# Optimization experiments

Hardware: AMD Instinct MI355X
Metric: run time of the kernel (lower is better)

Reference implementation:

```python
import jax, jax.numpy as jnp
import numpy as np

HEAD_DIM = 64
N_HEADS = 64
N_KV = 8
Q_MULT = N_HEADS // N_KV  # 8
HIDDEN = 2880
SLIDING_WINDOW = 128
BASE = 150000.0
INIT_CTX = 4096
SCALING = 32.0
NTK_ALPHA = 1.0   # beta_slow
NTK_BETA = 32.0   # beta_fast
EPS = 1e-5
SM_SCALE = 1.0 / np.sqrt(HEAD_DIM)


def _cos_sin(num_tokens):
    # YaRN-style NTK rope (scaling_factor > 1 branch)
    freq = BASE ** (jnp.arange(0, HEAD_DIM, 2, dtype=jnp.float32) / HEAD_DIM)
    concentration = 0.1 * np.log(SCALING) + 1.0
    d_half = HEAD_DIM // 2
    low = d_half * np.log(INIT_CTX / (NTK_BETA * 2 * np.pi)) / np.log(BASE)
    high = d_half * np.log(INIT_CTX / (NTK_ALPHA * 2 * np.pi)) / np.log(BASE)
    interpolation = 1.0 / (SCALING * freq)
    extrapolation = 1.0 / freq
    ramp = (jnp.arange(d_half, dtype=jnp.float32) - low) / (high - low)
    mask = 1.0 - jnp.clip(ramp, 0.0, 1.0)
    inv_freq = interpolation * (1.0 - mask) + extrapolation * mask
    t = jnp.arange(num_tokens, dtype=jnp.float32)
    freqs = t[:, None] * inv_freq[None, :]  # [n, d/2]
    return jnp.cos(freqs) * concentration, jnp.sin(freqs) * concentration


def _apply_rotary(x, cos, sin):
    # x: [n, h, d]; cos/sin: [n, d/2]
    cos = cos[:, None, :].astype(x.dtype)
    sin = sin[:, None, :].astype(x.dtype)
    x1, x2 = jnp.split(x, 2, axis=-1)
    return jnp.concatenate((x1 * cos - x2 * sin, x2 * cos + x1 * sin), axis=-1)


def _forward(x, norm_w, qkv_w, out_w, sinks):
    b, s, h = x.shape  # b=1
    n = b * s
    # RMSNorm
    var = jnp.mean(jnp.square(x), axis=-1, keepdims=True)
    t = x * jax.lax.rsqrt(var + EPS) * norm_w
    # QKV projection
    qkv = jnp.einsum('bsh,hf->bsf', t, qkv_w)
    q_dim = N_HEADS * HEAD_DIM
    kv_dim = N_KV * HEAD_DIM
    q = qkv[:, :, :q_dim].reshape(n, N_KV, Q_MULT, HEAD_DIM)
    k = qkv[:, :, q_dim:q_dim + kv_dim].reshape(n, N_KV, HEAD_DIM)
    v = qkv[:, :, q_dim + kv_dim:].reshape(n, N_KV, HEAD_DIM)
    # RoPE
    cos, sin = _cos_sin(n)
    q = _apply_rotary(q.reshape(n, -1, HEAD_DIM), cos, sin).reshape(n, N_KV, Q_MULT, HEAD_DIM)
    k = _apply_rotary(k, cos, sin)
    # sdpa with sliding window + sink logits
    qk = jnp.einsum('qhmd,khd->hmqk', q, k) * SM_SCALE  # [N_KV, Q_MULT, n, n]
    i = jnp.arange(n)[:, None]
    j = jnp.arange(n)[None, :]
    neg_inf = jnp.array(-jnp.inf, dtype=qk.dtype)
    banned = (j > i) | (i - j >= SLIDING_WINDOW)  # causal + sliding window
    qk = jnp.where(banned[None, None, :, :], neg_inf, qk)
    S = jnp.broadcast_to(sinks.reshape(N_KV, Q_MULT, 1, 1), (N_KV, Q_MULT, n, 1))
    logits = jnp.concatenate([qk, S], axis=-1)  # [N_KV, Q_MULT, n, n+1]
    w = jax.nn.softmax(logits, axis=-1)[..., :-1]
    attn = jnp.einsum('hmqk,khd->qhmd', w, v).reshape(n, N_HEADS * HEAD_DIM)
    out = jnp.einsum('qf,fh->qh', attn, out_w)  # [n, hidden]
    return x + out  # broadcasts to [b, s, hidden]


def setup_inputs() -> dict:
    key = jax.random.key(0)
    k1, k2, k3, k4, k5 = jax.random.split(key, 5)
    x = jax.random.normal(k1, (1, 2048, HIDDEN), dtype=jnp.float32)
    norm_w = jax.random.uniform(k2, (HIDDEN,), dtype=jnp.float32, minval=0.5, maxval=1.5)
    qkv_w = jax.random.normal(k3, (HIDDEN, HEAD_DIM * (N_HEADS + 2 * N_KV)), dtype=jnp.float32) * 0.02
    out_w = jax.random.normal(k4, (HEAD_DIM * N_HEADS, HIDDEN), dtype=jnp.float32) * 0.02
    sinks = jax.random.normal(k5, (N_HEADS,), dtype=jnp.float32)
    return {"x": x, "norm_w": norm_w, "qkv_w": qkv_w, "out_w": out_w, "sinks": sinks}


def reference(x, norm_w, qkv_w, out_w, sinks):
    return _forward(x, norm_w, qkv_w, out_w, sinks)
```

## Files before the change

### kernel.cpp

```cpp
#include <hip/hip_runtime.h>
#include <math.h>

typedef unsigned short u16;
typedef unsigned int u32;
typedef short bf4 __attribute__((ext_vector_type(4)));
typedef __bf16 bfv8 __attribute__((ext_vector_type(8)));
typedef float f4 __attribute__((ext_vector_type(4)));

#define SEQ 2048
#define HID 2880
#define KPAD 2944
#define QKVN 5120

static __device__ __forceinline__ u16 f2bf(float x) {
  union { float f; u32 u; } v; v.f = x;
  u32 r = v.u + 0x7fffu + ((v.u >> 16) & 1u);
  return (u16)(r >> 16);
}
static __device__ __forceinline__ float bf2f(u16 s) {
  union { u32 u; float f; } v; v.u = ((u32)s) << 16;
  return v.f;
}
static __device__ __forceinline__ void gl_lds16(const void* g, void* l) {
  __builtin_amdgcn_global_load_lds((const __attribute__((address_space(1))) u32*)g,
                                   (__attribute__((address_space(3))) u32*)l, 16, 0, 0);
}
#define MFMA(a, b, c) __builtin_amdgcn_mfma_f32_16x16x16bf16_1k(a, b, c, 0, 0, 0)
#define MFMA32(a, b, c) __builtin_amdgcn_mfma_f32_16x16x32_bf16(a, b, c, 0, 0, 0)
#define BAR __builtin_amdgcn_s_barrier()
#define SCHEDB __builtin_amdgcn_sched_barrier(0)
#define VMCNT0 asm volatile("s_waitcnt vmcnt(0)" ::: "memory")
#define LGKM0 asm volatile("s_waitcnt lgkmcnt(0)" ::: "memory")
#define LGKM2 asm volatile("s_waitcnt lgkmcnt(2)" ::: "memory")

__global__ __launch_bounds__(256) void k_rmsnorm(const float* __restrict__ x,
                                                 const float* __restrict__ w,
                                                 u16* __restrict__ t) {
  const int row = blockIdx.x;
  const float* xr = x + (size_t)row * HID;
  float ss = 0.f;
  for (int i = threadIdx.x; i < 720; i += 256) {
    float4 v = ((const float4*)xr)[i];
    ss += v.x * v.x + v.y * v.y + v.z * v.z + v.w * v.w;
  }
#pragma unroll
  for (int m = 1; m < 64; m <<= 1) ss += __shfl_xor(ss, m);
  __shared__ float red[4];
  if ((threadIdx.x & 63) == 0) red[threadIdx.x >> 6] = ss;
  __syncthreads();
  float sc = rsqrtf((red[0] + red[1] + red[2] + red[3]) * (1.0f / HID) + 1e-5f);
  u16* tr = t + (size_t)row * KPAD;
  for (int i = threadIdx.x; i < 720; i += 256) {
    float4 v = ((const float4*)xr)[i];
    float4 wv = ((const float4*)w)[i];
    ushort4 o;
    o.x = f2bf(v.x * sc * wv.x);
    o.y = f2bf(v.y * sc * wv.y);
    o.z = f2bf(v.z * sc * wv.z);
    o.w = f2bf(v.w * sc * wv.w);
    ((ushort4*)tr)[i] = o;
  }
  if (threadIdx.x < 16) ((ushort4*)tr)[720 + threadIdx.x] = make_ushort4(0, 0, 0, 0);
}

__global__ __launch_bounds__(256) void k_convT(const float* __restrict__ W,
                                               u16* __restrict__ WT, int K, int Kpad,
                                               int Nsrc) {
  __shared__ u16 tile[64][65];
  const int n0 = blockIdx.x * 64, k0 = blockIdx.y * 64;
  for (int s = threadIdx.x; s < 1024; s += 256) {
    int r = s >> 4, c4 = (s & 15) * 4;
    int kk = k0 + r, nn = n0 + c4;
    float4 v = make_float4(0.f, 0.f, 0.f, 0.f);
    if (kk < K && nn < Nsrc) v = *(const float4*)&W[(size_t)kk * Nsrc + nn];
    tile[c4 + 0][r] = f2bf(v.x);
    tile[c4 + 1][r] = f2bf(v.y);
    tile[c4 + 2][r] = f2bf(v.z);
    tile[c4 + 3][r] = f2bf(v.w);
  }
  __syncthreads();
  for (int s = threadIdx.x; s < 512; s += 256) {
    int r = s >> 3, c8 = (s & 7) * 8;
    u32 p0 = tile[r][c8 + 0] | ((u32)tile[r][c8 + 1] << 16);
    u32 p1 = tile[r][c8 + 2] | ((u32)tile[r][c8 + 3] << 16);
    u32 p2 = tile[r][c8 + 4] | ((u32)tile[r][c8 + 5] << 16);
    u32 p3 = tile[r][c8 + 6] | ((u32)tile[r][c8 + 7] << 16);
    *(uint4*)&WT[(size_t)(n0 + r) * Kpad + k0 + c8] = make_uint4(p0, p1, p2, p3);
  }
}

template <int MODE, int BN>
__global__ __launch_bounds__(512, 2) void k_gemm3(const u16* __restrict__ A,
                                                  const u16* __restrict__ BT,
                                                  void* __restrict__ Cv,
                                                  const float* __restrict__ resid,
                                                  int N, int Nout, int K) {
  constexpr int WN = BN / 4;
  constexpr int NF = WN / 16;
  constexpr int ABY = 128 * 128;
  constexpr int BBY = BN * 128;
  constexpr int TILE = ABY + BBY;
  constexpr int NB = BN / 64;
  __shared__ __align__(16) char lds[2 * TILE];
  const int n0 = blockIdx.x * BN, m0 = blockIdx.y * 128;
  const int tid = threadIdx.x;
  const int l = tid & 63, w = tid >> 6;
  const int wm = w >> 2, wn = w & 3;
  const int g = l >> 4, q = l & 15;
  const int NT = K >> 6;
  const int srow = tid >> 3;
  const int sc8 = ((tid & 7) ^ (srow & 7)) * 8;

#define STAGE_A(bo, kt, qa) gl_lds16(A + (size_t)(m0 + (qa)*64 + srow) * K + (kt)*64 + sc8, \
    lds + (bo) + (qa)*8192 + tid*16)
#define STAGE_B(bo, kt, qb) gl_lds16(BT + (size_t)(n0 + (qb)*64 + srow) * K + (kt)*64 + sc8, \
    lds + (bo) + ABY + (qb)*8192 + tid*16)
#define LDB2(dst, nf) { const int r = wn * WN + (nf)*16 + q; \
    dst[0] = *(const bfv8*)(lds + bo + ABY + r * 128 + (((g) ^ (r & 7)) << 4)); \
    dst[1] = *(const bfv8*)(lds + bo + ABY + r * 128 + (((4 + g) ^ (r & 7)) << 4)); }

  f4 acc[4][NF] = {};
#pragma unroll
  for (int qa = 0; qa < 2; ++qa) STAGE_A(0, 0, qa);
#pragma unroll
  for (int qb = 0; qb < NB; ++qb) STAGE_B(0, 0, qb);
  VMCNT0; SCHEDB; BAR;

  for (int t = 0; t < NT; ++t) {
    const int bo = (t & 1) * TILE;
    const int so = bo ^ TILE;
    if (t + 1 < NT) {
#pragma unroll
      for (int qa = 0; qa < 2; ++qa) STAGE_A(so, t + 1, qa);
#pragma unroll
      for (int qb = 0; qb < NB; ++qb) STAGE_B(so, t + 1, qb);
    }
    SCHEDB;
    bfv8 af[4][2], bb[2][2];
#pragma unroll
    for (int mf = 0; mf < 4; ++mf) {
      const int r = wm * 64 + mf * 16 + q;
      af[mf][0] = *(const bfv8*)(lds + bo + r * 128 + (((g) ^ (r & 7)) << 4));
      af[mf][1] = *(const bfv8*)(lds + bo + r * 128 + (((4 + g) ^ (r & 7)) << 4));
    }
    LDB2(bb[0], 0);
    SCHEDB;
    LDB2(bb[1], 1);
    __builtin_amdgcn_s_setprio(1);
#pragma unroll
    for (int nf = 0; nf < NF; ++nf) {
      if (nf == NF - 1) { LGKM0; } else { LGKM2; }
      SCHEDB;
#pragma unroll
      for (int mf = 0; mf < 4; ++mf) {
        acc[mf][nf] = MFMA32(af[mf][0], bb[nf & 1][0], acc[mf][nf]);
        acc[mf][nf] = MFMA32(af[mf][1], bb[nf & 1][1], acc[mf][nf]);
      }
      if (nf + 2 < NF) LDB2(bb[nf & 1], nf + 2);
    }
    __builtin_amdgcn_s_setprio(0);
    VMCNT0;
    SCHEDB; BAR;
  }
#pragma unroll
  for (int mf = 0; mf < 4; ++mf)
#pragma unroll
    for (int nf = 0; nf < NF; ++nf)
#pragma unroll
      for (int r = 0; r < 4; ++r) {
        int row = m0 + wm * 64 + mf * 16 + g * 4 + r;
        int col = n0 + wn * WN + nf * 16 + q;
        if constexpr (MODE == 0) {
          ((u16*)Cv)[(size_t)row * N + col] = f2bf(acc[mf][nf][r]);
        } else {
          if (col < Nout)
            ((float*)Cv)[(size_t)row * Nout + col] =
                acc[mf][nf][r] + resid[(size_t)row * Nout + col];
        }
      }
#undef STAGE_A
#undef STAGE_B
#undef LDB2
}

__global__ __launch_bounds__(256) void k_rope(u16* __restrict__ qkv) {
  __shared__ float lcs[64];
  const int t = blockIdx.x;
  if (threadIdx.x < 32) {
    const int d = threadIdx.x;
    const float low = 8.0927791f, high = 17.3980236f, conc = 1.3465735903f;
    float freq = powf(150000.0f, (float)d * (1.0f / 32.0f));
    float r01 = fminf(fmaxf(((float)d - low) / (high - low), 0.f), 1.f);
    float invf = (1.0f / (32.0f * freq)) * r01 + (1.0f / freq) * (1.f - r01);
    float ang = (float)t * invf;
    lcs[d] = cosf(ang) * conc;
    lcs[d + 32] = sinf(ang) * conc;
  }
  __syncthreads();
  for (int i = threadIdx.x; i < 2304; i += 256) {
    const int d = i & 31, hd = i >> 5;
    u16* base = qkv + (size_t)t * QKVN + (hd < 64 ? hd * 64 : 4096 + (hd - 64) * 64);
    float cc = lcs[d], ss = lcs[d + 32];
    float x1 = bf2f(base[d]), x2 = bf2f(base[d + 32]);
    base[d] = f2bf(x1 * cc - x2 * ss);
    base[d + 32] = f2bf(x2 * cc + x1 * ss);
  }
}

__global__ __launch_bounds__(256) void k_vtrans(const u16* __restrict__ qkv,
                                                u16* __restrict__ vt) {
  __shared__ u16 tile[64][72];
  const int t0 = blockIdx.x * 64, h = blockIdx.y;
  for (int s = threadIdx.x; s < 512; s += 256) {
    int r = s >> 3, c8 = (s & 7) * 8;
    uint4 v = *(const uint4*)&qkv[(size_t)(t0 + r) * QKVN + 4608 + h * 64 + c8];
    *(uint4*)&tile[r][c8] = v;
  }
  __syncthreads();
  for (int s = threadIdx.x; s < 512; s += 256) {
    int d = s >> 3, c8 = (s & 7) * 8;
    u32 p0 = tile[c8 + 0][d] | ((u32)tile[c8 + 1][d] << 16);
    u32 p1 = tile[c8 + 2][d] | ((u32)tile[c8 + 3][d] << 16);
    u32 p2 = tile[c8 + 4][d] | ((u32)tile[c8 + 5][d] << 16);
    u32 p3 = tile[c8 + 6][d] | ((u32)tile[c8 + 7][d] << 16);
    *(uint4*)&vt[((size_t)h * 64 + d) * SEQ + t0 + c8] = make_uint4(p0, p1, p2, p3);
  }
}

__global__ __launch_bounds__(512) void k_attn(const u16* __restrict__ qkv,
                                              const u16* __restrict__ vt,
                                              const float* __restrict__ sinks,
                                              u16* __restrict__ attn) {
  __shared__ u16 lK[144 * 72];
  __shared__ u16 lV[64 * 152];
  __shared__ u16 lP[8 * 16 * 148];
  const int t0 = blockIdx.x * 16;
  const int h = blockIdx.y;
  const int j0 = t0 - 128;
  const int tid = threadIdx.x;
  for (int s = tid; s < 1152; s += 512) {
    int row = s >> 3, c = s & 7;
    int j = j0 + row;
    uint4 v = make_uint4(0, 0, 0, 0);
    if (j >= 0) v = *(const uint4*)&qkv[(size_t)j * QKVN + 4096 + h * 64 + c * 8];
    *(uint4*)&lK[row * 72 + c * 8] = v;
  }
  for (int s = tid; s < 1152; s += 512) {
    int d = s / 18, c = s - d * 18;
    int jb = j0 + c * 8;
    uint4 v = make_uint4(0, 0, 0, 0);
    if (jb >= 0) v = *(const uint4*)&vt[((size_t)h * 64 + d) * SEQ + jb];
    *(uint4*)&lV[d * 152 + c * 8] = v;
  }
  __syncthreads();
  const int w = tid >> 6, l = tid & 63;
  const int g = l >> 4, q = l & 15;
  const int hq = h * 8 + w;
  const float sink = sinks[hq];
  bf4 qf[4];
  const u16* qrow = qkv + (size_t)(t0 + q) * QKVN + hq * 64;
#pragma unroll
  for (int ks = 0; ks < 4; ++ks) qf[ks] = *(const bf4*)&qrow[ks * 16 + g * 4];
  f4 sacc[9];
#pragma unroll
  for (int nt = 0; nt < 9; ++nt) {
    f4 z = {0.f, 0.f, 0.f, 0.f};
    sacc[nt] = z;
#pragma unroll
    for (int ks = 0; ks < 4; ++ks) {
      bf4 kf = *(const bf4*)&lK[(nt * 16 + q) * 72 + ks * 16 + g * 4];
      sacc[nt] = MFMA(qf[ks], kf, sacc[nt]);
    }
  }
  const float NEG = -__builtin_inff();
  float rmax[4] = {NEG, NEG, NEG, NEG};
#pragma unroll
  for (int nt = 0; nt < 9; ++nt)
#pragma unroll
    for (int r = 0; r < 4; ++r) {
      float sv = sacc[nt][r] * 0.125f;
      int it = t0 + g * 4 + r;
      int j = j0 + nt * 16 + q;
      bool ban = (j > it) || (it - j >= 128) || (j < 0);
      sv = ban ? NEG : sv;
      sacc[nt][r] = sv;
      rmax[r] = fmaxf(rmax[r], sv);
    }
#pragma unroll
  for (int r = 0; r < 4; ++r)
#pragma unroll
    for (int m = 1; m < 16; m <<= 1) rmax[r] = fmaxf(rmax[r], __shfl_xor(rmax[r], m));
  float ssum[4];
  u16* pbase = lP + w * (16 * 148);
#pragma unroll
  for (int r = 0; r < 4; ++r) {
    float mf = fmaxf(rmax[r], sink);
    float ps = 0.f;
#pragma unroll
    for (int nt = 0; nt < 9; ++nt) {
      float p = __expf(sacc[nt][r] - mf);
      pbase[(g * 4 + r) * 148 + nt * 16 + q] = f2bf(p);
      ps += p;
    }
#pragma unroll
    for (int m = 1; m < 16; m <<= 1) ps += __shfl_xor(ps, m);
    ssum[r] = ps + __expf(sink - mf);
  }
  f4 oacc[4] = {};
#pragma unroll
  for (int kt = 0; kt < 9; ++kt) {
    bf4 pa = *(const bf4*)&pbase[q * 148 + kt * 16 + g * 4];
#pragma unroll
    for (int nt = 0; nt < 4; ++nt) {
      bf4 vf = *(const bf4*)&lV[(nt * 16 + q) * 152 + kt * 16 + g * 4];
      oacc[nt] = MFMA(pa, vf, oacc[nt]);
    }
  }
#pragma unroll
  for (int nt = 0; nt < 4; ++nt)
#pragma unroll
    for (int r = 0; r < 4; ++r) {
      int row = t0 + g * 4 + r;
      attn[(size_t)row * 4096 + hq * 64 + nt * 16 + q] = f2bf(oacc[nt][r] / ssum[r]);
    }
}

extern "C" void kernel_launch(void* const* d_in, const int* in_sizes, int n_in,
                              void* d_out, int out_size, void* d_ws, size_t ws_size,
                              hipStream_t stream) {
  const float* x = (const float*)d_in[0];
  const float* norm_w = (const float*)d_in[1];
  const float* qkv_w = (const float*)d_in[2];
  const float* out_w = (const float*)d_in[3];
  const float* sinks = (const float*)d_in[4];
  float* out = (float*)d_out;
  char* ws = (char*)d_ws;
  u16* t     = (u16*)(ws);
  u16* wqkvT = (u16*)(ws + 12058624);
  u16* qkv   = (u16*)(ws + 42205184);
  u16* vt    = (u16*)(ws + 63176704);
  u16* woutT = (u16*)(ws + 65273856);
  u16* attnO = (u16*)(ws);

  k_rmsnorm<<<dim3(2048), dim3(256), 0, stream>>>(x, norm_w, t);
  k_convT<<<dim3(80, 46), dim3(256), 0, stream>>>(qkv_w, wqkvT, 2880, KPAD, 5120);
  k_convT<<<dim3(48, 64), dim3(256), 0, stream>>>(out_w, woutT, 4096, 4096, 2880);
  k_gemm3<0, 320><<<dim3(16, 16), dim3(512), 0, stream>>>(t, wqkvT, (void*)qkv,
                                                          nullptr, 5120, 5120, KPAD);
  k_rope<<<dim3(2048), dim3(256), 0, stream>>>(qkv);
  k_vtrans<<<dim3(32, 8), dim3(256), 0, stream>>>(qkv, vt);
  k_attn<<<dim3(128, 8), dim3(512), 0, stream>>>(qkv, vt, sinks, attnO);
  k_gemm3<1, 192><<<dim3(16, 16), dim3(512), 0, stream>>>(attnO, woutT, (void*)out,
                                                          x, 3072, 2880, 4096);
}
```

Measured before the change: 185.2 us.

## Prefetch next tile's LDS fragments across barrier with double-buffered registers in GEMM

Restructures the GEMM main loop into a two-tile unrolled body with ping-pong register fragment sets. After the barrier, the next tile's A/B fragments are loaded from LDS while the last N-fragment MFMAs of the current tile run, hiding LDS read latency at the tile boundary. This doubles fragment registers, so launch bounds drop to one block per CU, reducing occupancy. The loop assumes an even tile count (NT=46 and 64 both even).

```diff
diff --git a/kernel.cpp b/kernel.cpp
--- a/kernel.cpp
+++ b/kernel.cpp
@@ -32,6 +32,7 @@
 #define VMCNT0 asm volatile("s_waitcnt vmcnt(0)" ::: "memory")
 #define LGKM0 asm volatile("s_waitcnt lgkmcnt(0)" ::: "memory")
 #define LGKM2 asm volatile("s_waitcnt lgkmcnt(2)" ::: "memory")
+#define LGKM12 asm volatile("s_waitcnt lgkmcnt(12)" ::: "memory")
 
 __global__ __launch_bounds__(256) void k_rmsnorm(const float* __restrict__ x,
                                                  const float* __restrict__ w,
@@ -90,7 +91,7 @@
 }
 
 template <int MODE, int BN>
-__global__ __launch_bounds__(512, 2) void k_gemm3(const u16* __restrict__ A,
+__global__ __launch_bounds__(512, 1) void k_gemm4(const u16* __restrict__ A,
                                                   const u16* __restrict__ BT,
                                                   void* __restrict__ Cv,
                                                   const float* __restrict__ resid,
@@ -115,52 +116,68 @@
     lds + (bo) + (qa)*8192 + tid*16)
 #define STAGE_B(bo, kt, qb) gl_lds16(BT + (size_t)(n0 + (qb)*64 + srow) * K + (kt)*64 + sc8, \
     lds + (bo) + ABY + (qb)*8192 + tid*16)
-#define LDB2(dst, nf) { const int r = wn * WN + (nf)*16 + q; \
-    dst[0] = *(const bfv8*)(lds + bo + ABY + r * 128 + (((g) ^ (r & 7)) << 4)); \
-    dst[1] = *(const bfv8*)(lds + bo + ABY + r * 128 + (((4 + g) ^ (r & 7)) << 4)); }
+#define LDB2(DST, nf_, bo_) { const int r_ = wn * WN + (nf_)*16 + q; \
+    DST[0] = *(const bfv8*)(lds + (bo_) + ABY + r_ * 128 + (((g) ^ (r_ & 7)) << 4)); \
+    DST[1] = *(const bfv8*)(lds + (bo_) + ABY + r_ * 128 + (((4 + g) ^ (r_ & 7)) << 4)); }
+#define LDA8(AF, bo_) { _Pragma("unroll") for (int mf = 0; mf < 4; ++mf) { \
+    const int r_ = wm * 64 + mf * 16 + q; \
+    AF[mf][0] = *(const bfv8*)(lds + (bo_) + r_ * 128 + (((g) ^ (r_ & 7)) << 4)); \
+    AF[mf][1] = *(const bfv8*)(lds + (bo_) + r_ * 128 + (((4 + g) ^ (r_ & 7)) << 4)); } }
+#define CHUNK(nf_, AFC, BB_) { LGKM2; SCHEDB; \
+    _Pragma("unroll") for (int mf = 0; mf < 4; ++mf) { \
+      acc[mf][nf_] = MFMA32(AFC[mf][0], BB_[0], acc[mf][nf_]); \
+      acc[mf][nf_] = MFMA32(AFC[mf][1], BB_[1], acc[mf][nf_]); } }
+
+#define TILE_BODY(t_, bo_, so_, AFC, B0C, B1C, AFN, B0N, B1N) { \
+    const int t__ = (t_); \
+    const bool pf__ = (t__ + 1 < NT); \
+    if (pf__) { \
+      _Pragma("unroll") for (int qa = 0; qa < 2; ++qa) STAGE_A(so_, t__ + 1, qa); \
+      _Pragma("unroll") for (int qb = 0; qb < NB; ++qb) STAGE_B(so_, t__ + 1, qb); \
+    } \
+    SCHEDB; \
+    __builtin_amdgcn_s_setprio(1); \
+    CHUNK(0, AFC, B0C); LDB2(B0C, 2, bo_); \
+    CHUNK(1, AFC, B1C); \
+    if constexpr (NF == 5) { \
+      LDB2(B1C, 3, bo_); \
+      CHUNK(2, AFC, B0C); LDB2(B0C, 4, bo_); \
+      CHUNK(3, AFC, B1C); \
+    } \
+    __builtin_amdgcn_s_setprio(0); \
+    VMCNT0; SCHEDB; BAR; SCHEDB; \
+    if (pf__) { \
+      LDA8(AFN, so_); \
+      LDB2(B0N, 0, so_); \
+      LDB2(B1N, 1, so_); \
+    } \
+    __builtin_amdgcn_s_setprio(1); \
+    if (pf__) { LGKM12; } else { LGKM0; } \
+    SCHEDB; \
+    _Pragma("unroll") for (int mf = 0; mf < 4; ++mf) { \
+      acc[mf][NF - 1] = MFMA32(AFC[mf][0], B0C[0], acc[mf][NF - 1]); \
+      acc[mf][NF - 1] = MFMA32(AFC[mf][1], B0C[1], acc[mf][NF - 1]); \
+    } \
+    __builtin_amdgcn_s_setprio(0); \
+    SCHEDB; BAR; \
+  }
 
   f4 acc[4][NF] = {};
+  bfv8 afP[4][2], afQ[4][2];
+  bfv8 b0P[2], b1P[2], b0Q[2], b1Q[2];
+
 #pragma unroll
   for (int qa = 0; qa < 2; ++qa) STAGE_A(0, 0, qa);
 #pragma unroll
   for (int qb = 0; qb < NB; ++qb) STAGE_B(0, 0, qb);
-  VMCNT0; SCHEDB; BAR;
-
-  for (int t = 0; t < NT; ++t) {
-    const int bo = (t & 1) * TILE;
-    const int so = bo ^ TILE;
-    if (t + 1 < NT) {
-#pragma unroll
-      for (int qa = 0; qa < 2; ++qa) STAGE_A(so, t + 1, qa);
-#pragma unroll
-      for (int qb = 0; qb < NB; ++qb) STAGE_B(so, t + 1, qb);
-    }
-    SCHEDB;
-    bfv8 af[4][2], bb[2][2];
-#pragma unroll
-    for (int mf = 0; mf < 4; ++mf) {
-      const int r = wm * 64 + mf * 16 + q;
-      af[mf][0] = *(const bfv8*)(lds + bo + r * 128 + (((g) ^ (r & 7)) << 4));
-      af[mf][1] = *(const bfv8*)(lds + bo + r * 128 + (((4 + g) ^ (r & 7)) << 4));
-    }
-    LDB2(bb[0], 0);
-    SCHEDB;
-    LDB2(bb[1], 1);
-    __builtin_amdgcn_s_setprio(1);
-#pragma unroll
-    for (int nf = 0; nf < NF; ++nf) {
-      if (nf == NF - 1) { LGKM0; } else { LGKM2; }
-      SCHEDB;
-#pragma unroll
-      for (int mf = 0; mf < 4; ++mf) {
-        acc[mf][nf] = MFMA32(af[mf][0], bb[nf & 1][0], acc[mf][nf]);
-        acc[mf][nf] = MFMA32(af[mf][1], bb[nf & 1][1], acc[mf][nf]);
-      }
-      if (nf + 2 < NF) LDB2(bb[nf & 1], nf + 2);
-    }
-    __builtin_amdgcn_s_setprio(0);
-    VMCNT0;
-    SCHEDB; BAR;
+  VMCNT0; SCHEDB; BAR; SCHEDB;
+  LDA8(afP, 0);
+  LDB2(b0P, 0, 0);
+  LDB2(b1P, 1, 0);
+
+  for (int t = 0; t + 1 < NT; t += 2) {
+    TILE_BODY(t,     0,    TILE, afP, b0P, b1P, afQ, b0Q, b1Q);
+    TILE_BODY(t + 1, TILE, 0,    afQ, b0Q, b1Q, afP, b0P, b1P);
   }
 #pragma unroll
   for (int mf = 0; mf < 4; ++mf)
@@ -181,6 +198,9 @@
 #undef STAGE_A
 #undef STAGE_B
 #undef LDB2
+#undef LDA8
+#undef CHUNK
+#undef TILE_BODY
 }
 
 __global__ __launch_bounds__(256) void k_rope(u16* __restrict__ qkv) {
@@ -345,11 +365,11 @@
   k_rmsnorm<<<dim3(2048), dim3(256), 0, stream>>>(x, norm_w, t);
   k_convT<<<dim3(80, 46), dim3(256), 0, stream>>>(qkv_w, wqkvT, 2880, KPAD, 5120);
   k_convT<<<dim3(48, 64), dim3(256), 0, stream>>>(out_w, woutT, 4096, 4096, 2880);
-  k_gemm3<0, 320><<<dim3(16, 16), dim3(512), 0, stream>>>(t, wqkvT, (void*)qkv,
+  k_gemm4<0, 320><<<dim3(16, 16), dim3(512), 0, stream>>>(t, wqkvT, (void*)qkv,
                                                           nullptr, 5120, 5120, KPAD);
   k_rope<<<dim3(2048), dim3(256), 0, stream>>>(qkv);
   k_vtrans<<<dim3(32, 8), dim3(256), 0, stream>>>(qkv, vt);
   k_attn<<<dim3(128, 8), dim3(512), 0, stream>>>(qkv, vt, sinks, attnO);
-  k_gemm3<1, 192><<<dim3(16, 16), dim3(512), 0, stream>>>(attnO, woutT, (void*)out,
+  k_gemm4<1, 192><<<dim3(16, 16), dim3(512), 0, stream>>>(attnO, woutT, (void*)out,
                                                           x, 3072, 2880, 4096);
 }
```

Result: slower. 205.7 us (+11.1%).

## Restructure GEMMs to 2-wave blocks with 128-row warp tiles

Applied to the files above, without the earlier changes.

Both projection GEMMs move from 512-thread blocks (8 waves, 64x(BN/4) warp tiles) to 128-thread blocks with 2 waves. Each wave now covers all 128 rows and half of the block's columns, and block column width is halved so the grid doubles to 32x16. All 8 A fragments are loaded per k-step with a staggered lgkmcnt wait schedule, so MFMAs start as soon as each fragment arrives. This raises register reuse of B fragments per wave. In exchange there are far fewer waves per CU, which risks latency hiding, and many more accumulator registers are needed.

```diff
diff --git a/kernel.cpp b/kernel.cpp
--- a/kernel.cpp
+++ b/kernel.cpp
@@ -30,8 +30,7 @@
 #define BAR __builtin_amdgcn_s_barrier()
 #define SCHEDB __builtin_amdgcn_sched_barrier(0)
 #define VMCNT0 asm volatile("s_waitcnt vmcnt(0)" ::: "memory")
-#define LGKM0 asm volatile("s_waitcnt lgkmcnt(0)" ::: "memory")
-#define LGKM2 asm volatile("s_waitcnt lgkmcnt(2)" ::: "memory")
+#define LGKMN(n) asm volatile("s_waitcnt lgkmcnt(" #n ")" ::: "memory")
 
 __global__ __launch_bounds__(256) void k_rmsnorm(const float* __restrict__ x,
                                                  const float* __restrict__ w,
@@ -90,40 +89,50 @@
 }
 
 template <int MODE, int BN>
-__global__ __launch_bounds__(512, 2) void k_gemm3(const u16* __restrict__ A,
+__global__ __launch_bounds__(128, 1) void k_gemm5(const u16* __restrict__ A,
                                                   const u16* __restrict__ BT,
                                                   void* __restrict__ Cv,
                                                   const float* __restrict__ resid,
                                                   int N, int Nout, int K) {
-  constexpr int WN = BN / 4;
+  constexpr int WN = BN / 2;
   constexpr int NF = WN / 16;
   constexpr int ABY = 128 * 128;
   constexpr int BBY = BN * 128;
   constexpr int TILE = ABY + BBY;
-  constexpr int NB = BN / 64;
+  constexpr int NBC = BBY / 2048;
   __shared__ __align__(16) char lds[2 * TILE];
   const int n0 = blockIdx.x * BN, m0 = blockIdx.y * 128;
   const int tid = threadIdx.x;
   const int l = tid & 63, w = tid >> 6;
-  const int wm = w >> 2, wn = w & 3;
   const int g = l >> 4, q = l & 15;
   const int NT = K >> 6;
-  const int srow = tid >> 3;
-  const int sc8 = ((tid & 7) ^ (srow & 7)) * 8;
-
-#define STAGE_A(bo, kt, qa) gl_lds16(A + (size_t)(m0 + (qa)*64 + srow) * K + (kt)*64 + sc8, \
-    lds + (bo) + (qa)*8192 + tid*16)
-#define STAGE_B(bo, kt, qb) gl_lds16(BT + (size_t)(n0 + (qb)*64 + srow) * K + (kt)*64 + sc8, \
-    lds + (bo) + ABY + (qb)*8192 + tid*16)
-#define LDB2(dst, nf) { const int r = wn * WN + (nf)*16 + q; \
-    dst[0] = *(const bfv8*)(lds + bo + ABY + r * 128 + (((g) ^ (r & 7)) << 4)); \
-    dst[1] = *(const bfv8*)(lds + bo + ABY + r * 128 + (((4 + g) ^ (r & 7)) << 4)); }
-
-  f4 acc[4][NF] = {};
-#pragma unroll
-  for (int qa = 0; qa < 2; ++qa) STAGE_A(0, 0, qa);
-#pragma unroll
-  for (int qb = 0; qb < NB; ++qb) STAGE_B(0, 0, qb);
+
+#define STAGE_A(bo, kt, p) { const int slot = (p)*128 + tid; \
+    const int row = slot >> 3, c = slot & 7; \
+    gl_lds16(A + (size_t)(m0 + row) * K + (kt)*64 + ((c ^ (row & 7)) * 8), \
+             lds + (bo) + slot * 16); }
+#define STAGE_B(bo, kt, p) { const int slot = (p)*128 + tid; \
+    const int row = slot >> 3, c = slot & 7; \
+    gl_lds16(BT + (size_t)(n0 + row) * K + (kt)*64 + ((c ^ (row & 7)) * 8), \
+             lds + (bo) + ABY + slot * 16); }
+#define LDB2(DST, nf_, bo_) { const int r_ = w * WN + (nf_)*16 + q; \
+    DST[0] = *(const bfv8*)(lds + (bo_) + ABY + r_ * 128 + (((g) ^ (r_ & 7)) << 4)); \
+    DST[1] = *(const bfv8*)(lds + (bo_) + ABY + r_ * 128 + (((4 + g) ^ (r_ & 7)) << 4)); }
+#define LDA2(mf_, bo_) { const int r_ = (mf_)*16 + q; \
+    af[mf_][0] = *(const bfv8*)(lds + (bo_) + r_ * 128 + (((g) ^ (r_ & 7)) << 4)); \
+    af[mf_][1] = *(const bfv8*)(lds + (bo_) + r_ * 128 + (((4 + g) ^ (r_ & 7)) << 4)); }
+#define MF2(mf_, nf_, BB_) { \
+    acc[mf_][nf_] = MFMA32(af[mf_][0], BB_[0], acc[mf_][nf_]); \
+    acc[mf_][nf_] = MFMA32(af[mf_][1], BB_[1], acc[mf_][nf_]); }
+#define ENT(mf_, n_) { LGKMN(n_); SCHEDB; MF2(mf_, 0, bb[0]); }
+
+  f4 acc[8][NF] = {};
+  bfv8 af[8][2], bb[2][2];
+
+#pragma unroll
+  for (int p = 0; p < 8; ++p) STAGE_A(0, 0, p);
+#pragma unroll
+  for (int p = 0; p < NBC; ++p) STAGE_B(0, 0, p);
   VMCNT0; SCHEDB; BAR;
 
   for (int t = 0; t < NT; ++t) {
@@ -131,45 +140,40 @@
     const int so = bo ^ TILE;
     if (t + 1 < NT) {
 #pragma unroll
-      for (int qa = 0; qa < 2; ++qa) STAGE_A(so, t + 1, qa);
-#pragma unroll
-      for (int qb = 0; qb < NB; ++qb) STAGE_B(so, t + 1, qb);
+      for (int p = 0; p < 8; ++p) STAGE_A(so, t + 1, p);
+#pragma unroll
+      for (int p = 0; p < NBC; ++p) STAGE_B(so, t + 1, p);
     }
     SCHEDB;
-    bfv8 af[4][2], bb[2][2];
-#pragma unroll
-    for (int mf = 0; mf < 4; ++mf) {
-      const int r = wm * 64 + mf * 16 + q;
-      af[mf][0] = *(const bfv8*)(lds + bo + r * 128 + (((g) ^ (r & 7)) << 4));
-      af[mf][1] = *(const bfv8*)(lds + bo + r * 128 + (((4 + g) ^ (r & 7)) << 4));
-    }
-    LDB2(bb[0], 0);
-    SCHEDB;
-    LDB2(bb[1], 1);
+    LDB2(bb[0], 0, bo); SCHEDB;
+    LDA2(0, bo); SCHEDB; LDA2(1, bo); SCHEDB;
+    LDA2(2, bo); SCHEDB; LDA2(3, bo); SCHEDB;
+    LDA2(4, bo); SCHEDB; LDA2(5, bo); SCHEDB;
+    LDA2(6, bo); SCHEDB; LDA2(7, bo); SCHEDB;
+    LDB2(bb[1], 1, bo); SCHEDB;
     __builtin_amdgcn_s_setprio(1);
-#pragma unroll
-    for (int nf = 0; nf < NF; ++nf) {
-      if (nf == NF - 1) { LGKM0; } else { LGKM2; }
+    ENT(0, 15) ENT(1, 14) ENT(2, 12) ENT(3, 10)
+    ENT(4, 8)  ENT(5, 6)  ENT(6, 4)  ENT(7, 2)
+#pragma unroll
+    for (int nf = 1; nf < NF; ++nf) {
+      if (nf + 1 < NF) { LDB2(bb[(nf + 1) & 1], nf + 1, bo); LGKMN(2); }
+      else             { LGKMN(0); }
       SCHEDB;
 #pragma unroll
-      for (int mf = 0; mf < 4; ++mf) {
-        acc[mf][nf] = MFMA32(af[mf][0], bb[nf & 1][0], acc[mf][nf]);
-        acc[mf][nf] = MFMA32(af[mf][1], bb[nf & 1][1], acc[mf][nf]);
-      }
-      if (nf + 2 < NF) LDB2(bb[nf & 1], nf + 2);
+      for (int mf = 0; mf < 8; ++mf) MF2(mf, nf, bb[nf & 1]);
     }
     __builtin_amdgcn_s_setprio(0);
     VMCNT0;
     SCHEDB; BAR;
   }
 #pragma unroll
-  for (int mf = 0; mf < 4; ++mf)
+  for (int mf = 0; mf < 8; ++mf)
 #pragma unroll
     for (int nf = 0; nf < NF; ++nf)
 #pragma unroll
       for (int r = 0; r < 4; ++r) {
-        int row = m0 + wm * 64 + mf * 16 + g * 4 + r;
-        int col = n0 + wn * WN + nf * 16 + q;
+        int row = m0 + mf * 16 + g * 4 + r;
+        int col = n0 + w * WN + nf * 16 + q;
         if constexpr (MODE == 0) {
           ((u16*)Cv)[(size_t)row * N + col] = f2bf(acc[mf][nf][r]);
         } else {
@@ -181,6 +185,9 @@
 #undef STAGE_A
 #undef STAGE_B
 #undef LDB2
+#undef LDA2
+#undef MF2
+#undef ENT
 }
 
 __global__ __launch_bounds__(256) void k_rope(u16* __restrict__ qkv) {
@@ -345,11 +352,11 @@
   k_rmsnorm<<<dim3(2048), dim3(256), 0, stream>>>(x, norm_w, t);
   k_convT<<<dim3(80, 46), dim3(256), 0, stream>>>(qkv_w, wqkvT, 2880, KPAD, 5120);
   k_convT<<<dim3(48, 64), dim3(256), 0, stream>>>(out_w, woutT, 4096, 4096, 2880);
-  k_gemm3<0, 320><<<dim3(16, 16), dim3(512), 0, stream>>>(t, wqkvT, (void*)qkv,
+  k_gemm5<0, 160><<<dim3(32, 16), dim3(128), 0, stream>>>(t, wqkvT, (void*)qkv,
                                                           nullptr, 5120, 5120, KPAD);
   k_rope<<<dim3(2048), dim3(256), 0, stream>>>(qkv);
   k_vtrans<<<dim3(32, 8), dim3(256), 0, stream>>>(qkv, vt);
   k_attn<<<dim3(128, 8), dim3(512), 0, stream>>>(qkv, vt, sinks, attnO);
-  k_gemm3<1, 192><<<dim3(16, 16), dim3(512), 0, stream>>>(attnO, woutT, (void*)out,
-                                                          x, 3072, 2880, 4096);
-}
+  k_gemm5<1, 96><<<dim3(32, 16), dim3(128), 0, stream>>>(attnO, woutT, (void*)out,
+                                                         x, 3072, 2880, 4096);
+}
```

After: 204.4 us. 10.4% more time.
